# Kernel optimization log

Measured on AMD Instinct MI355X. Metric: run time of the kernel, lower is better.

Reference implementation:

```python
import jax, jax.numpy as jnp
import numpy as np

BETA = 0.25


def setup_inputs() -> dict:
    key = jax.random.key(0)
    k1, k2 = jax.random.split(key)
    z = jax.random.normal(k1, (16, 64, 64, 64), dtype=jnp.float32)        # [B, e_dim, H, W]
    codebook = jax.random.normal(k2, (2048, 64), dtype=jnp.float32)       # [n_e, e_dim]
    return {"z": z, "codebook": codebook}


def reference(z, codebook):
    B, C, H, W = z.shape
    n_e = codebook.shape[0]
    sg = jax.lax.stop_gradient

    zp = jnp.transpose(z, (0, 2, 3, 1))                # [B, H, W, C]
    zf = zp.reshape(-1, C)                             # [N, C]

    # nearest-code logits (inner product; CE in source is dead code)
    logits = zf @ codebook.T                           # [N, n_e]
    idx = jnp.argmax(logits, axis=1)                   # [N]

    z_q = codebook[idx].reshape(zp.shape)              # [B, H, W, C]

    # commitment + codebook loss (this overwrites the CE loss in the source)
    loss = BETA * jnp.mean((sg(z_q) - zp) ** 2) + jnp.mean((z_q - sg(zp)) ** 2)

    # straight-through estimator
    z_q_st = zp + sg(z_q - zp)

    # perplexity via one-hot mean (scatter-add instead of dense one-hot)
    counts = jnp.zeros((n_e,), dtype=zp.dtype).at[idx].add(1.0)
    e_mean = counts / idx.shape[0]
    perplexity = jnp.exp(-jnp.sum(e_mean * jnp.log(e_mean + 1e-10)))

    indices = idx.reshape(B, H * W).astype(jnp.int32)
    z_q_out = jnp.transpose(z_q_st, (0, 3, 1, 2))      # back to [B, C, H, W]
    return z_q_out, loss, perplexity, indices
```

## Files before the change

### kernel.cpp

```cpp
#include <hip/hip_runtime.h>

#define C_DIM   64
#define HW      4096
#define NROWS   65536
#define N_E     2048
#define N_ELEM  4194304
#define OUT_LOSS_OFF 4194304
#define OUT_PPL_OFF  4194305
#define OUT_IDX_OFF  4194306

#define ROWS_B   128
#define NTILE    (N_E / 16)
#define TILE_F4  384

typedef __attribute__((ext_vector_type(8))) short bf16x8;
typedef __attribute__((ext_vector_type(4))) float f32x4;

__device__ __forceinline__ unsigned short f2bf(float f) {
    unsigned u = __float_as_uint(f);
    return (unsigned short)((u + 0x7FFFu + ((u >> 16) & 1u)) >> 16);
}
__device__ __forceinline__ float bf2f(unsigned short b) {
    return __uint_as_float(((unsigned)b) << 16);
}

__global__ __launch_bounds__(256) void vq_prep(
    const float* __restrict__ cb, unsigned short* __restrict__ cbp)
{
    const int u = blockIdx.x * 256 + threadIdx.x;
    const int c = u >> 6, k = u & 63;
    const float v = cb[u];
    const unsigned short s1 = f2bf(v);
    const float r1 = v - bf2f(s1);
    const unsigned short s2 = f2bf(r1);
    const float r2 = r1 - bf2f(s2);
    const unsigned short s3 = f2bf(r2);
    const int tile = c >> 4, k2 = k >> 5, kk = k & 31;
    const int lane = (kk >> 3) * 16 + (c & 15), i = kk & 7;
    const int base = ((tile * 3 + 0) * 2 + k2) * 512 + lane * 8 + i;
    cbp[base]        = s1;
    cbp[base + 1024] = s2;
    cbp[base + 2048] = s3;
}

#define M16(A_, B_, C_) __builtin_amdgcn_mfma_f32_16x16x32_bf16((A_), (B_), (C_), 0, 0, 0)

#define PASS8(ACC, NT)                                                         \
    ACC = M16(A[0][0], zf[0][NT][0], ACC); ACC = M16(A[0][1], zf[0][NT][1], ACC); \
    ACC = M16(A[0][0], zf[1][NT][0], ACC); ACC = M16(A[0][1], zf[1][NT][1], ACC); \
    ACC = M16(A[1][0], zf[0][NT][0], ACC); ACC = M16(A[1][1], zf[0][NT][1], ACC); \
    ACC = M16(A[1][0], zf[1][NT][0], ACC); ACC = M16(A[1][1], zf[1][NT][1], ACC); \
    ACC = M16(A[0][0], zf[2][NT][0], ACC); ACC = M16(A[0][1], zf[2][NT][1], ACC); \
    ACC = M16(A[2][0], zf[0][NT][0], ACC); ACC = M16(A[2][1], zf[0][NT][1], ACC); \
    ACC = M16(A[1][0], zf[2][NT][0], ACC); ACC = M16(A[1][1], zf[2][NT][1], ACC); \
    ACC = M16(A[2][0], zf[1][NT][0], ACC); ACC = M16(A[2][1], zf[1][NT][1], ACC);

__global__ __launch_bounds__(256, 2) void vq_mfma(
    const float* __restrict__ z, const float* __restrict__ cb,
    const unsigned short* __restrict__ cbp, float* __restrict__ out,
    int* __restrict__ counts, float* __restrict__ loss_accum)
{
    __shared__ __align__(16) float zs[C_DIM][ROWS_B];
    __shared__ float4 cbbuf[2][TILE_F4];
    __shared__ int    sidx[ROWS_B];
    __shared__ float  wsum[4];

    const int tid  = threadIdx.x;
    const int lane = tid & 63;
    const int wv   = tid >> 6;
    const int l15  = lane & 15, lg = lane >> 4;
    const int row0 = blockIdx.x * ROWS_B;
    const int b    = row0 >> 12;
    const int hw0  = row0 & 4095;
    const float* zb = z + (size_t)b * C_DIM * HW + hw0;

#pragma unroll
    for (int j = 0; j < 8; ++j) {
        const int u = j * 256 + tid;
        const int c = u >> 5, x4 = u & 31;
        float4 v = *(const float4*)(zb + (size_t)c * HW + x4 * 4);
        *(float4*)&zs[c][x4 * 4] = v;
    }
    const float4* cbp4 = (const float4*)cbp;
    {
        float4 p0 = cbp4[tid];
        cbbuf[0][tid] = p0;
        if (tid < 128) { float4 p1 = cbp4[256 + tid]; cbbuf[0][256 + tid] = p1; }
    }
    __syncthreads();

    bf16x8 zf[3][2][2];
#pragma unroll
    for (int nt = 0; nt < 2; ++nt) {
        const int row_l = wv * 32 + nt * 16 + l15;
#pragma unroll
        for (int k2 = 0; k2 < 2; ++k2) {
#pragma unroll
            for (int i = 0; i < 8; ++i) {
                float v = zs[k2 * 32 + lg * 8 + i][row_l];
                unsigned short s1 = f2bf(v);
                float r1 = v - bf2f(s1);
                unsigned short s2 = f2bf(r1);
                float r2 = r1 - bf2f(s2);
                zf[0][nt][k2][i] = (short)s1;
                zf[1][nt][k2][i] = (short)s2;
                zf[2][nt][k2][i] = (short)f2bf(r2);
            }
        }
    }

    float best0 = -3.4e38f, best1 = -3.4e38f;
    int   bi0 = 0, bi1 = 0;
    const f32x4 zero4 = {0.f, 0.f, 0.f, 0.f};

    for (int t = 0; t < NTILE; ++t) {
        float4 q0 = {0,0,0,0}, q1 = {0,0,0,0};
        if (t + 1 < NTILE) {
            q0 = cbp4[(size_t)(t + 1) * TILE_F4 + tid];
            if (tid < 128) q1 = cbp4[(size_t)(t + 1) * TILE_F4 + 256 + tid];
        }
        const bf16x8* Ab = (const bf16x8*)&cbbuf[t & 1][0];
        bf16x8 A[3][2];
#pragma unroll
        for (int s = 0; s < 3; ++s)
#pragma unroll
            for (int k2 = 0; k2 < 2; ++k2)
                A[s][k2] = Ab[(s * 2 + k2) * 64 + lane];

        f32x4 acc0 = zero4, acc1 = zero4;
        PASS8(acc0, 0)
        PASS8(acc1, 1)

        const int cbase = t * 16 + lg * 4;
#pragma unroll
        for (int r = 0; r < 4; ++r) {
            if (acc0[r] > best0) { best0 = acc0[r]; bi0 = cbase + r; }
            if (acc1[r] > best1) { best1 = acc1[r]; bi1 = cbase + r; }
        }

        if (t + 1 < NTILE) {
            cbbuf[(t + 1) & 1][tid] = q0;
            if (tid < 128) cbbuf[(t + 1) & 1][256 + tid] = q1;
        }
        __syncthreads();
    }

#pragma unroll
    for (int off = 16; off <= 32; off <<= 1) {
        float ob = __shfl_xor(best0, off, 64); int oi = __shfl_xor(bi0, off, 64);
        if (ob > best0 || (ob == best0 && oi < bi0)) { best0 = ob; bi0 = oi; }
        ob = __shfl_xor(best1, off, 64); oi = __shfl_xor(bi1, off, 64);
        if (ob > best1 || (ob == best1 && oi < bi1)) { best1 = ob; bi1 = oi; }
    }
    if (lane < 32) {
        const int nt = lane >> 4;
        const int row_l = wv * 32 + lane;
        const int ii = (nt == 0) ? bi0 : bi1;
        sidx[row_l] = ii;
        out[OUT_IDX_OFF + row0 + row_l] = (float)ii;
        atomicAdd(&counts[ii], 1);
    }
    __syncthreads();

    float lsum = 0.f;
#pragma unroll
    for (int j = 0; j < 8; ++j) {
        const int m = j * 256 + tid;
        const int r = m & 127, c4 = m >> 7;
        const float4 q4 = *(const float4*)(cb + (size_t)sidx[r] * C_DIM + c4 * 4);
#pragma unroll
        for (int q = 0; q < 4; ++q) {
            const int c = c4 * 4 + q;
            const float zv = zs[c][r];
            const float qv = (q == 0) ? q4.x : (q == 1) ? q4.y : (q == 2) ? q4.z : q4.w;
            const float d = qv - zv;
            lsum += d * d;
            out[(size_t)b * C_DIM * HW + (size_t)c * HW + hw0 + r] = zv + d;
        }
    }
    for (int off = 32; off > 0; off >>= 1) lsum += __shfl_down(lsum, off, 64);
    if (lane == 0) wsum[wv] = lsum;
    __syncthreads();
    if (tid == 0)
        atomicAdd(loss_accum, wsum[0] + wsum[1] + wsum[2] + wsum[3]);
}

__global__ __launch_bounds__(256) void vq_finalize(
    const int* __restrict__ counts, const float* __restrict__ loss_accum,
    float* __restrict__ out)
{
    float h = 0.f;
    for (int e = threadIdx.x; e < N_E; e += 256) {
        float em = (float)counts[e] * (1.0f / (float)NROWS);
        h -= em * logf(em + 1e-10f);
    }
    for (int off = 32; off > 0; off >>= 1) h += __shfl_down(h, off, 64);
    __shared__ float hs[4];
    const int lane = threadIdx.x & 63, w = threadIdx.x >> 6;
    if (lane == 0) hs[w] = h;
    __syncthreads();
    if (threadIdx.x == 0) {
        float H = hs[0] + hs[1] + hs[2] + hs[3];
        float m = loss_accum[0] * (1.0f / (float)N_ELEM);
        out[OUT_LOSS_OFF] = 0.25f * m + m;
        out[OUT_PPL_OFF]  = expf(H);
    }
}

extern "C" void kernel_launch(void* const* d_in, const int* in_sizes, int n_in,
                              void* d_out, int out_size, void* d_ws, size_t ws_size,
                              hipStream_t stream)
{
    const float* z  = (const float*)d_in[0];
    const float* cb = (const float*)d_in[1];
    float* out = (float*)d_out;

    int*            counts     = (int*)d_ws;
    float*          loss_accum = (float*)((char*)d_ws + N_E * sizeof(int));
    unsigned short* cbp        = (unsigned short*)((char*)d_ws + 16384);

    hipMemsetAsync(counts, 0, N_E * sizeof(int) + sizeof(float), stream);

    vq_prep<<<N_E * C_DIM / 256, 256, 0, stream>>>(cb, cbp);
    vq_mfma<<<NROWS / ROWS_B, 256, 0, stream>>>(z, cb, cbp, out, counts, loss_accum);
    vq_finalize<<<1, 256, 0, stream>>>(counts, loss_accum, out);
}
```

Measured before the change: 174.8 us.

## Double rows per block, register-prefetch codebook fragments, drop memset and z smem staging

Each block now handles 256 rows (64 per wave), so every codebook tile loaded into LDS feeds twice as many MFMAs. The codebook LDS pipeline prefetches two tiles ahead, and the next tile's fragments are read into registers before the current tile's MFMAs run. z is no longer staged in shared memory; it is read directly from global memory, both for the bf16 split and in the epilogue. The memset is folded into the prep kernel. The costs are higher register pressure, which may reduce occupancy, half as many blocks (256), and strided direct global reads of z.

```diff
diff --git a/kernel.cpp b/kernel.cpp
--- a/kernel.cpp
+++ b/kernel.cpp
@@ -9,7 +9,7 @@
 #define OUT_PPL_OFF  4194305
 #define OUT_IDX_OFF  4194306
 
-#define ROWS_B   128
+#define ROWS_B   256
 #define NTILE    (N_E / 16)
 #define TILE_F4  384
 
@@ -25,9 +25,12 @@
 }
 
 __global__ __launch_bounds__(256) void vq_prep(
-    const float* __restrict__ cb, unsigned short* __restrict__ cbp)
+    const float* __restrict__ cb, unsigned short* __restrict__ cbp,
+    int* __restrict__ counts, float* __restrict__ loss_accum)
 {
     const int u = blockIdx.x * 256 + threadIdx.x;
+    if (u < N_E) counts[u] = 0;
+    if (u == 0)  *loss_accum = 0.f;
     const int c = u >> 6, k = u & 63;
     const float v = cb[u];
     const unsigned short s1 = f2bf(v);
@@ -45,22 +48,22 @@
 
 #define M16(A_, B_, C_) __builtin_amdgcn_mfma_f32_16x16x32_bf16((A_), (B_), (C_), 0, 0, 0)
 
-#define PASS8(ACC, NT)                                                         \
-    ACC = M16(A[0][0], zf[0][NT][0], ACC); ACC = M16(A[0][1], zf[0][NT][1], ACC); \
-    ACC = M16(A[0][0], zf[1][NT][0], ACC); ACC = M16(A[0][1], zf[1][NT][1], ACC); \
-    ACC = M16(A[1][0], zf[0][NT][0], ACC); ACC = M16(A[1][1], zf[0][NT][1], ACC); \
-    ACC = M16(A[1][0], zf[1][NT][0], ACC); ACC = M16(A[1][1], zf[1][NT][1], ACC); \
-    ACC = M16(A[0][0], zf[2][NT][0], ACC); ACC = M16(A[0][1], zf[2][NT][1], ACC); \
-    ACC = M16(A[2][0], zf[0][NT][0], ACC); ACC = M16(A[2][1], zf[0][NT][1], ACC); \
-    ACC = M16(A[1][0], zf[2][NT][0], ACC); ACC = M16(A[1][1], zf[2][NT][1], ACC); \
-    ACC = M16(A[2][0], zf[1][NT][0], ACC); ACC = M16(A[2][1], zf[1][NT][1], ACC);
+#define PASS8(AA, ACC, NT)                                                      \
+    ACC = M16(AA[0], zf[0][NT][0], ACC); ACC = M16(AA[1], zf[0][NT][1], ACC);   \
+    ACC = M16(AA[0], zf[1][NT][0], ACC); ACC = M16(AA[1], zf[1][NT][1], ACC);   \
+    ACC = M16(AA[2], zf[0][NT][0], ACC); ACC = M16(AA[3], zf[0][NT][1], ACC);   \
+    ACC = M16(AA[2], zf[1][NT][0], ACC); ACC = M16(AA[3], zf[1][NT][1], ACC);   \
+    ACC = M16(AA[0], zf[2][NT][0], ACC); ACC = M16(AA[1], zf[2][NT][1], ACC);   \
+    ACC = M16(AA[4], zf[0][NT][0], ACC); ACC = M16(AA[5], zf[0][NT][1], ACC);   \
+    ACC = M16(AA[2], zf[2][NT][0], ACC); ACC = M16(AA[3], zf[2][NT][1], ACC);   \
+    ACC = M16(AA[4], zf[1][NT][0], ACC); ACC = M16(AA[5], zf[1][NT][1], ACC);
+
 
 __global__ __launch_bounds__(256, 2) void vq_mfma(
     const float* __restrict__ z, const float* __restrict__ cb,
     const unsigned short* __restrict__ cbp, float* __restrict__ out,
     int* __restrict__ counts, float* __restrict__ loss_accum)
 {
-    __shared__ __align__(16) float zs[C_DIM][ROWS_B];
     __shared__ float4 cbbuf[2][TILE_F4];
     __shared__ int    sidx[ROWS_B];
     __shared__ float  wsum[4];
@@ -74,30 +77,15 @@
     const int hw0  = row0 & 4095;
     const float* zb = z + (size_t)b * C_DIM * HW + hw0;
 
-#pragma unroll
-    for (int j = 0; j < 8; ++j) {
-        const int u = j * 256 + tid;
-        const int c = u >> 5, x4 = u & 31;
-        float4 v = *(const float4*)(zb + (size_t)c * HW + x4 * 4);
-        *(float4*)&zs[c][x4 * 4] = v;
-    }
-    const float4* cbp4 = (const float4*)cbp;
-    {
-        float4 p0 = cbp4[tid];
-        cbbuf[0][tid] = p0;
-        if (tid < 128) { float4 p1 = cbp4[256 + tid]; cbbuf[0][256 + tid] = p1; }
-    }
-    __syncthreads();
-
-    bf16x8 zf[3][2][2];
-#pragma unroll
-    for (int nt = 0; nt < 2; ++nt) {
-        const int row_l = wv * 32 + nt * 16 + l15;
+    bf16x8 zf[3][4][2];
+#pragma unroll
+    for (int nt = 0; nt < 4; ++nt) {
+        const int row_l = wv * 64 + nt * 16 + l15;
 #pragma unroll
         for (int k2 = 0; k2 < 2; ++k2) {
 #pragma unroll
             for (int i = 0; i < 8; ++i) {
-                float v = zs[k2 * 32 + lg * 8 + i][row_l];
+                float v = zb[(size_t)(k2 * 32 + lg * 8 + i) * HW + row_l];
                 unsigned short s1 = f2bf(v);
                 float r1 = v - bf2f(s1);
                 unsigned short s2 = f2bf(r1);
@@ -109,73 +97,104 @@
         }
     }
 
-    float best0 = -3.4e38f, best1 = -3.4e38f;
-    int   bi0 = 0, bi1 = 0;
+    const float4* cbp4 = (const float4*)cbp;
+#pragma unroll
+    for (int tt = 0; tt < 2; ++tt) {
+        float4 p0 = cbp4[(size_t)tt * TILE_F4 + tid];
+        cbbuf[tt][tid] = p0;
+        if (tid < 128) {
+            float4 p1 = cbp4[(size_t)tt * TILE_F4 + 256 + tid];
+            cbbuf[tt][256 + tid] = p1;
+        }
+    }
+    __syncthreads();
+
+    bf16x8 Acur[6], Anxt[6];
+    {
+        const bf16x8* Ab = (const bf16x8*)&cbbuf[0][0];
+#pragma unroll
+        for (int f = 0; f < 6; ++f) Acur[f] = Ab[f * 64 + lane];
+    }
+
+    float best0 = -3.4e38f, best1 = -3.4e38f, best2 = -3.4e38f, best3 = -3.4e38f;
+    int   bi0 = 0, bi1 = 0, bi2 = 0, bi3 = 0;
     const f32x4 zero4 = {0.f, 0.f, 0.f, 0.f};
 
+#pragma unroll 1
     for (int t = 0; t < NTILE; ++t) {
         float4 q0 = {0,0,0,0}, q1 = {0,0,0,0};
+        const bool pf = (t + 2 < NTILE);
+        if (pf) {
+            q0 = cbp4[(size_t)(t + 2) * TILE_F4 + tid];
+            if (tid < 128) q1 = cbp4[(size_t)(t + 2) * TILE_F4 + 256 + tid];
+        }
         if (t + 1 < NTILE) {
-            q0 = cbp4[(size_t)(t + 1) * TILE_F4 + tid];
-            if (tid < 128) q1 = cbp4[(size_t)(t + 1) * TILE_F4 + 256 + tid];
-        }
-        const bf16x8* Ab = (const bf16x8*)&cbbuf[t & 1][0];
-        bf16x8 A[3][2];
-#pragma unroll
-        for (int s = 0; s < 3; ++s)
-#pragma unroll
-            for (int k2 = 0; k2 < 2; ++k2)
-                A[s][k2] = Ab[(s * 2 + k2) * 64 + lane];
-
-        f32x4 acc0 = zero4, acc1 = zero4;
-        PASS8(acc0, 0)
-        PASS8(acc1, 1)
+            const bf16x8* Ab = (const bf16x8*)&cbbuf[(t + 1) & 1][0];
+#pragma unroll
+            for (int f = 0; f < 6; ++f) Anxt[f] = Ab[f * 64 + lane];
+        }
+
+        f32x4 acc0 = zero4, acc1 = zero4, acc2 = zero4, acc3 = zero4;
+        PASS8(Acur, acc0, 0)
+        PASS8(Acur, acc1, 1)
+        PASS8(Acur, acc2, 2)
+        PASS8(Acur, acc3, 3)
 
         const int cbase = t * 16 + lg * 4;
 #pragma unroll
         for (int r = 0; r < 4; ++r) {
             if (acc0[r] > best0) { best0 = acc0[r]; bi0 = cbase + r; }
             if (acc1[r] > best1) { best1 = acc1[r]; bi1 = cbase + r; }
-        }
-
+            if (acc2[r] > best2) { best2 = acc2[r]; bi2 = cbase + r; }
+            if (acc3[r] > best3) { best3 = acc3[r]; bi3 = cbase + r; }
+        }
+
+        if (pf) {
+            cbbuf[t & 1][tid] = q0;
+            if (tid < 128) cbbuf[t & 1][256 + tid] = q1;
+        }
+        __syncthreads();
         if (t + 1 < NTILE) {
-            cbbuf[(t + 1) & 1][tid] = q0;
-            if (tid < 128) cbbuf[(t + 1) & 1][256 + tid] = q1;
-        }
-        __syncthreads();
+#pragma unroll
+            for (int f = 0; f < 6; ++f) Acur[f] = Anxt[f];
+        }
     }
 
 #pragma unroll
     for (int off = 16; off <= 32; off <<= 1) {
-        float ob = __shfl_xor(best0, off, 64); int oi = __shfl_xor(bi0, off, 64);
+        float ob; int oi;
+        ob = __shfl_xor(best0, off, 64); oi = __shfl_xor(bi0, off, 64);
         if (ob > best0 || (ob == best0 && oi < bi0)) { best0 = ob; bi0 = oi; }
         ob = __shfl_xor(best1, off, 64); oi = __shfl_xor(bi1, off, 64);
         if (ob > best1 || (ob == best1 && oi < bi1)) { best1 = ob; bi1 = oi; }
-    }
-    if (lane < 32) {
-        const int nt = lane >> 4;
-        const int row_l = wv * 32 + lane;
-        const int ii = (nt == 0) ? bi0 : bi1;
+        ob = __shfl_xor(best2, off, 64); oi = __shfl_xor(bi2, off, 64);
+        if (ob > best2 || (ob == best2 && oi < bi2)) { best2 = ob; bi2 = oi; }
+        ob = __shfl_xor(best3, off, 64); oi = __shfl_xor(bi3, off, 64);
+        if (ob > best3 || (ob == best3 && oi < bi3)) { best3 = ob; bi3 = oi; }
+    }
+    {
+        const int ii = (lg == 0) ? bi0 : (lg == 1) ? bi1 : (lg == 2) ? bi2 : bi3;
+        const int row_l = wv * 64 + lane;
         sidx[row_l] = ii;
         out[OUT_IDX_OFF + row0 + row_l] = (float)ii;
         atomicAdd(&counts[ii], 1);
     }
     __syncthreads();
 
+    float* ob0 = out + (size_t)b * C_DIM * HW + hw0;
     float lsum = 0.f;
 #pragma unroll
-    for (int j = 0; j < 8; ++j) {
-        const int m = j * 256 + tid;
-        const int r = m & 127, c4 = m >> 7;
-        const float4 q4 = *(const float4*)(cb + (size_t)sidx[r] * C_DIM + c4 * 4);
+    for (int j = 0; j < 16; ++j) {
+        const int c4 = j;
+        const float4 q4 = *(const float4*)(cb + (size_t)sidx[tid] * C_DIM + c4 * 4);
 #pragma unroll
         for (int q = 0; q < 4; ++q) {
             const int c = c4 * 4 + q;
-            const float zv = zs[c][r];
+            const float zv = zb[(size_t)c * HW + tid];
             const float qv = (q == 0) ? q4.x : (q == 1) ? q4.y : (q == 2) ? q4.z : q4.w;
             const float d = qv - zv;
             lsum += d * d;
-            out[(size_t)b * C_DIM * HW + (size_t)c * HW + hw0 + r] = zv + d;
+            ob0[(size_t)c * HW + tid] = zv + d;
         }
     }
     for (int off = 32; off > 0; off >>= 1) lsum += __shfl_down(lsum, off, 64);
@@ -219,9 +238,7 @@
     float*          loss_accum = (float*)((char*)d_ws + N_E * sizeof(int));
     unsigned short* cbp        = (unsigned short*)((char*)d_ws + 16384);
 
-    hipMemsetAsync(counts, 0, N_E * sizeof(int) + sizeof(float), stream);
-
-    vq_prep<<<N_E * C_DIM / 256, 256, 0, stream>>>(cb, cbp);
+    vq_prep<<<N_E * C_DIM / 256, 256, 0, stream>>>(cb, cbp, counts, loss_accum);
     vq_mfma<<<NROWS / ROWS_B, 256, 0, stream>>>(z, cb, cbp, out, counts, loss_accum);
     vq_finalize<<<1, 256, 0, stream>>>(counts, loss_accum, out);
 }
```

Measured after the change: 230.8 us. 1.32x slower.

## Load codebook fragments directly from global into registers, drop LDS staging

Applied to the files above, without the earlier changes.

The main loop no longer stages codebook tiles through double-buffered shared memory with a block barrier per tile. Each wave instead loads its bf16 fragments straight from global/L2 into registers, software-pipelined over two tiles. The z tile is also read from global instead of LDS, and the memset is folded into the prep kernel. This removes the 128 per-tile syncthreads and LDS traffic, and frees LDS for occupancy. In exchange every wave redundantly fetches the codebook from cache and z is read from global twice.

```diff
diff --git a/kernel.cpp b/kernel.cpp
--- a/kernel.cpp
+++ b/kernel.cpp
@@ -11,7 +11,7 @@
 
 #define ROWS_B   128
 #define NTILE    (N_E / 16)
-#define TILE_F4  384
+#define TILE_U   384
 
 typedef __attribute__((ext_vector_type(8))) short bf16x8;
 typedef __attribute__((ext_vector_type(4))) float f32x4;
@@ -25,9 +25,12 @@
 }
 
 __global__ __launch_bounds__(256) void vq_prep(
-    const float* __restrict__ cb, unsigned short* __restrict__ cbp)
+    const float* __restrict__ cb, unsigned short* __restrict__ cbp,
+    int* __restrict__ counts, float* __restrict__ loss_accum)
 {
     const int u = blockIdx.x * 256 + threadIdx.x;
+    if (u < N_E) counts[u] = 0;
+    if (u == 0)  *loss_accum = 0.f;
     const int c = u >> 6, k = u & 63;
     const float v = cb[u];
     const unsigned short s1 = f2bf(v);
@@ -45,25 +48,36 @@
 
 #define M16(A_, B_, C_) __builtin_amdgcn_mfma_f32_16x16x32_bf16((A_), (B_), (C_), 0, 0, 0)
 
-#define PASS8(ACC, NT)                                                         \
-    ACC = M16(A[0][0], zf[0][NT][0], ACC); ACC = M16(A[0][1], zf[0][NT][1], ACC); \
-    ACC = M16(A[0][0], zf[1][NT][0], ACC); ACC = M16(A[0][1], zf[1][NT][1], ACC); \
-    ACC = M16(A[1][0], zf[0][NT][0], ACC); ACC = M16(A[1][1], zf[0][NT][1], ACC); \
-    ACC = M16(A[1][0], zf[1][NT][0], ACC); ACC = M16(A[1][1], zf[1][NT][1], ACC); \
-    ACC = M16(A[0][0], zf[2][NT][0], ACC); ACC = M16(A[0][1], zf[2][NT][1], ACC); \
-    ACC = M16(A[2][0], zf[0][NT][0], ACC); ACC = M16(A[2][1], zf[0][NT][1], ACC); \
-    ACC = M16(A[1][0], zf[2][NT][0], ACC); ACC = M16(A[1][1], zf[2][NT][1], ACC); \
-    ACC = M16(A[2][0], zf[1][NT][0], ACC); ACC = M16(A[2][1], zf[1][NT][1], ACC);
+#define PASS8(AA, ACC, NT)                                                      \
+    ACC = M16(AA[0], zf[0][NT][0], ACC); ACC = M16(AA[1], zf[0][NT][1], ACC);   \
+    ACC = M16(AA[0], zf[1][NT][0], ACC); ACC = M16(AA[1], zf[1][NT][1], ACC);   \
+    ACC = M16(AA[2], zf[0][NT][0], ACC); ACC = M16(AA[3], zf[0][NT][1], ACC);   \
+    ACC = M16(AA[2], zf[1][NT][0], ACC); ACC = M16(AA[3], zf[1][NT][1], ACC);   \
+    ACC = M16(AA[0], zf[2][NT][0], ACC); ACC = M16(AA[1], zf[2][NT][1], ACC);   \
+    ACC = M16(AA[4], zf[0][NT][0], ACC); ACC = M16(AA[5], zf[0][NT][1], ACC);   \
+    ACC = M16(AA[2], zf[2][NT][0], ACC); ACC = M16(AA[3], zf[2][NT][1], ACC);   \
+    ACC = M16(AA[4], zf[1][NT][0], ACC); ACC = M16(AA[5], zf[1][NT][1], ACC);
+
+#define COMPUTE_TILE(T_, AA)                                                    \
+    {                                                                           \
+        f32x4 acc0 = zero4, acc1 = zero4;                                       \
+        PASS8(AA, acc0, 0)                                                      \
+        PASS8(AA, acc1, 1)                                                      \
+        const int cbase = (T_) * 16 + lg * 4;                                   \
+        _Pragma("unroll")                                                       \
+        for (int r = 0; r < 4; ++r) {                                           \
+            if (acc0[r] > best0) { best0 = acc0[r]; bi0 = cbase + r; }          \
+            if (acc1[r] > best1) { best1 = acc1[r]; bi1 = cbase + r; }          \
+        }                                                                       \
+    }
 
 __global__ __launch_bounds__(256, 2) void vq_mfma(
     const float* __restrict__ z, const float* __restrict__ cb,
     const unsigned short* __restrict__ cbp, float* __restrict__ out,
     int* __restrict__ counts, float* __restrict__ loss_accum)
 {
-    __shared__ __align__(16) float zs[C_DIM][ROWS_B];
-    __shared__ float4 cbbuf[2][TILE_F4];
-    __shared__ int    sidx[ROWS_B];
-    __shared__ float  wsum[4];
+    __shared__ int   sidx[ROWS_B];
+    __shared__ float wsum[4];
 
     const int tid  = threadIdx.x;
     const int lane = tid & 63;
@@ -74,21 +88,6 @@
     const int hw0  = row0 & 4095;
     const float* zb = z + (size_t)b * C_DIM * HW + hw0;
 
-#pragma unroll
-    for (int j = 0; j < 8; ++j) {
-        const int u = j * 256 + tid;
-        const int c = u >> 5, x4 = u & 31;
-        float4 v = *(const float4*)(zb + (size_t)c * HW + x4 * 4);
-        *(float4*)&zs[c][x4 * 4] = v;
-    }
-    const float4* cbp4 = (const float4*)cbp;
-    {
-        float4 p0 = cbp4[tid];
-        cbbuf[0][tid] = p0;
-        if (tid < 128) { float4 p1 = cbp4[256 + tid]; cbbuf[0][256 + tid] = p1; }
-    }
-    __syncthreads();
-
     bf16x8 zf[3][2][2];
 #pragma unroll
     for (int nt = 0; nt < 2; ++nt) {
@@ -97,7 +96,7 @@
         for (int k2 = 0; k2 < 2; ++k2) {
 #pragma unroll
             for (int i = 0; i < 8; ++i) {
-                float v = zs[k2 * 32 + lg * 8 + i][row_l];
+                float v = zb[(size_t)(k2 * 32 + lg * 8 + i) * HW + row_l];
                 unsigned short s1 = f2bf(v);
                 float r1 = v - bf2f(s1);
                 unsigned short s2 = f2bf(r1);
@@ -109,45 +108,36 @@
         }
     }
 
+    const bf16x8* cbpf = (const bf16x8*)cbp;
     float best0 = -3.4e38f, best1 = -3.4e38f;
     int   bi0 = 0, bi1 = 0;
     const f32x4 zero4 = {0.f, 0.f, 0.f, 0.f};
 
-    for (int t = 0; t < NTILE; ++t) {
-        float4 q0 = {0,0,0,0}, q1 = {0,0,0,0};
-        if (t + 1 < NTILE) {
-            q0 = cbp4[(size_t)(t + 1) * TILE_F4 + tid];
-            if (tid < 128) q1 = cbp4[(size_t)(t + 1) * TILE_F4 + 256 + tid];
+    bf16x8 Acur[6], Anxt[6];
+#pragma unroll
+    for (int f = 0; f < 6; ++f) Acur[f] = cbpf[f * 64 + lane];
+
+#pragma unroll 1
+    for (int t = 0; t < NTILE; t += 2) {
+#pragma unroll
+        for (int f = 0; f < 6; ++f)
+            Anxt[f] = cbpf[(size_t)(t + 1) * TILE_U + f * 64 + lane];
+
+        COMPUTE_TILE(t, Acur)
+
+        if (t + 2 < NTILE) {
+#pragma unroll
+            for (int f = 0; f < 6; ++f)
+                Acur[f] = cbpf[(size_t)(t + 2) * TILE_U + f * 64 + lane];
         }
-        const bf16x8* Ab = (const bf16x8*)&cbbuf[t & 1][0];
-        bf16x8 A[3][2];
-#pragma unroll
-        for (int s = 0; s < 3; ++s)
-#pragma unroll
-            for (int k2 = 0; k2 < 2; ++k2)
-                A[s][k2] = Ab[(s * 2 + k2) * 64 + lane];
-
-        f32x4 acc0 = zero4, acc1 = zero4;
-        PASS8(acc0, 0)
-        PASS8(acc1, 1)
-
-        const int cbase = t * 16 + lg * 4;
-#pragma unroll
-        for (int r = 0; r < 4; ++r) {
-            if (acc0[r] > best0) { best0 = acc0[r]; bi0 = cbase + r; }
-            if (acc1[r] > best1) { best1 = acc1[r]; bi1 = cbase + r; }
-        }
-
-        if (t + 1 < NTILE) {
-            cbbuf[(t + 1) & 1][tid] = q0;
-            if (tid < 128) cbbuf[(t + 1) & 1][256 + tid] = q1;
-        }
-        __syncthreads();
+
+        COMPUTE_TILE(t + 1, Anxt)
     }
 
 #pragma unroll
     for (int off = 16; off <= 32; off <<= 1) {
-        float ob = __shfl_xor(best0, off, 64); int oi = __shfl_xor(bi0, off, 64);
+        float ob; int oi;
+        ob = __shfl_xor(best0, off, 64); oi = __shfl_xor(bi0, off, 64);
         if (ob > best0 || (ob == best0 && oi < bi0)) { best0 = ob; bi0 = oi; }
         ob = __shfl_xor(best1, off, 64); oi = __shfl_xor(bi1, off, 64);
         if (ob > best1 || (ob == best1 && oi < bi1)) { best1 = ob; bi1 = oi; }
@@ -162,6 +152,7 @@
     }
     __syncthreads();
 
+    float* ob0 = out + (size_t)b * C_DIM * HW + hw0;
     float lsum = 0.f;
 #pragma unroll
     for (int j = 0; j < 8; ++j) {
@@ -171,11 +162,11 @@
 #pragma unroll
         for (int q = 0; q < 4; ++q) {
             const int c = c4 * 4 + q;
-            const float zv = zs[c][r];
+            const float zv = zb[(size_t)c * HW + r];
             const float qv = (q == 0) ? q4.x : (q == 1) ? q4.y : (q == 2) ? q4.z : q4.w;
             const float d = qv - zv;
             lsum += d * d;
-            out[(size_t)b * C_DIM * HW + (size_t)c * HW + hw0 + r] = zv + d;
+            ob0[(size_t)c * HW + r] = zv + d;
         }
     }
     for (int off = 32; off > 0; off >>= 1) lsum += __shfl_down(lsum, off, 64);
@@ -219,9 +210,7 @@
     float*          loss_accum = (float*)((char*)d_ws + N_E * sizeof(int));
     unsigned short* cbp        = (unsigned short*)((char*)d_ws + 16384);
 
-    hipMemsetAsync(counts, 0, N_E * sizeof(int) + sizeof(float), stream);
-
-    vq_prep<<<N_E * C_DIM / 256, 256, 0, stream>>>(cb, cbp);
+    vq_prep<<<N_E * C_DIM / 256, 256, 0, stream>>>(cb, cbp, counts, loss_accum);
     vq_mfma<<<NROWS / ROWS_B, 256, 0, stream>>>(z, cb, cbp, out, counts, loss_accum);
     vq_finalize<<<1, 256, 0, stream>>>(counts, loss_accum, out);
 }
```

New measurement: 170.1 us. 1.03x faster.
